# Performance work log

Measured on AMD Instinct MI355X. Metric: run time of the kernel, lower is better.

Reference implementation:

```python
import jax, jax.numpy as jnp
import numpy as np

B, S, D, H, DK, F, L, V = 4, 128, 512, 8, 64, 2048, 2, 32000
N = B * S  # nodes per side (enc and dec each)


def _pe():
    pos = np.arange(S, dtype=np.float32)[:, None]
    div = np.exp(-np.log(10000.0) * np.arange(0, D, 2, dtype=np.float32) / D)
    pe = np.zeros((S, D), dtype=np.float32)
    pe[:, 0::2] = np.sin(pos * div)
    pe[:, 1::2] = np.cos(pos * div)
    return jnp.asarray(np.tile(pe, (B, 1)))  # [N, D]


def _ln(x, g, b, eps=1e-5):
    mu = jnp.mean(x, -1, keepdims=True)
    var = jnp.mean(jnp.square(x - mu), -1, keepdims=True)
    return g * (x - mu) * jax.lax.rsqrt(var + eps) + b


def _edge_attn(q, k, v, src, dst, n_dst):
    # src_dot_dst('k','q','score') then scaled_exp, then src_mul_edge + sum scatter
    s = jnp.sum(k[src] * q[dst], -1, keepdims=True) / np.float32(np.sqrt(DK))  # [E,H,1]
    s = jnp.exp(jnp.clip(s, -10.0, 10.0))
    wv = jax.ops.segment_sum(v[src] * s, dst, num_segments=n_dst)  # [n_dst,H,DK]
    z = jax.ops.segment_sum(s, dst, num_segments=n_dst)            # [n_dst,H,1]
    return wv / z


def _attn_block(x_q, x_kv, Wq, Wk, Wv, Wo, src, dst):
    q = (x_q @ Wq).reshape(-1, H, DK)
    k = (x_kv @ Wk).reshape(-1, H, DK)
    v = (x_kv @ Wv).reshape(-1, H, DK)
    o = _edge_attn(q, k, v, src, dst, x_q.shape[0]).reshape(-1, D)
    return o @ Wo


def _forward(p, src_tok, tgt_tok, ee_src, ee_dst, dd_src, dd_dst, ed_src, ed_dst):
    (src_emb, tgt_emb, enc_Wqkv, enc_Wo, enc_ln1, enc_W1, enc_b1, enc_W2, enc_b2,
     enc_ln2, enc_lnf, dec_Wqkv, dec_Wo, dec_ln1, dec_cWq, dec_cWkv, dec_cWo,
     dec_ln2, dec_W1, dec_b1, dec_W2, dec_b2, dec_ln3, dec_lnf, gen_W, gen_b) = p
    pe = _pe()
    scale = np.float32(np.sqrt(D))
    x_e = src_emb[src_tok].reshape(N, D) * scale + pe  # token + positional embed
    x_d = tgt_emb[tgt_tok].reshape(N, D) * scale + pe
    for l in range(L):  # encoder layers (ee edges)
        xn = _ln(x_e, enc_ln1[l, 0], enc_ln1[l, 1])
        x_e = x_e + _attn_block(xn, xn, enc_Wqkv[l, 0], enc_Wqkv[l, 1], enc_Wqkv[l, 2], enc_Wo[l], ee_src, ee_dst)
        xn = _ln(x_e, enc_ln2[l, 0], enc_ln2[l, 1])
        x_e = x_e + jax.nn.relu(xn @ enc_W1[l] + enc_b1[l]) @ enc_W2[l] + enc_b2[l]
    x_e = _ln(x_e, enc_lnf[0], enc_lnf[1])
    for l in range(L):  # decoder layers: self (dd) then cross (ed)
        xn = _ln(x_d, dec_ln1[l, 0], dec_ln1[l, 1])
        x_d = x_d + _attn_block(xn, xn, dec_Wqkv[l, 0], dec_Wqkv[l, 1], dec_Wqkv[l, 2], dec_Wo[l], dd_src, dd_dst)
        xn = _ln(x_d, dec_ln2[l, 0], dec_ln2[l, 1])
        x_d = x_d + _attn_block(xn, x_e, dec_cWq[l], dec_cWkv[l, 0], dec_cWkv[l, 1], dec_cWo[l], ed_src, ed_dst)
        xn = _ln(x_d, dec_ln3[l, 0], dec_ln3[l, 1])
        x_d = x_d + jax.nn.relu(xn @ dec_W1[l] + dec_b1[l]) @ dec_W2[l] + dec_b2[l]
    x_d = _ln(x_d, dec_lnf[0], dec_lnf[1])
    return jax.nn.log_softmax(x_d @ gen_W + gen_b, axis=-1)  # generator


def setup_inputs():
    key = jax.random.key(0)
    ks = iter(jax.random.split(key, 32))
    w = lambda *shape: jax.random.normal(next(ks), shape, jnp.float32) * 0.02
    lnp = lambda n: jnp.tile(jnp.stack([jnp.ones(D), jnp.zeros(D)])[None], (n, 1, 1))
    # structured edge lists: per-sentence blocks
    i, j = np.meshgrid(np.arange(S), np.arange(S), indexing='ij')  # src pos, dst pos
    base = (np.arange(B)[:, None] * S).astype(np.int32)
    full_s = (base + i.ravel()[None, :]).ravel().astype(np.int32)
    full_d = (base + j.ravel()[None, :]).ravel().astype(np.int32)
    m = i.ravel() <= j.ravel()  # causal mask for dec self-attention
    dd_s = (base + i.ravel()[m][None, :]).ravel().astype(np.int32)
    dd_d = (base + j.ravel()[m][None, :]).ravel().astype(np.int32)
    k1, k2 = jax.random.split(next(ks))
    return dict(
        src_emb=w(V, D), tgt_emb=w(V, D),
        enc_Wqkv=w(L, 3, D, D), enc_Wo=w(L, D, D), enc_ln1=lnp(L),
        enc_W1=w(L, D, F), enc_b1=jnp.zeros((L, F)), enc_W2=w(L, F, D),
        enc_b2=jnp.zeros((L, D)), enc_ln2=lnp(L), enc_lnf=lnp(1)[0],
        dec_Wqkv=w(L, 3, D, D), dec_Wo=w(L, D, D), dec_ln1=lnp(L),
        dec_cWq=w(L, D, D), dec_cWkv=w(L, 2, D, D), dec_cWo=w(L, D, D), dec_ln2=lnp(L),
        dec_W1=w(L, D, F), dec_b1=jnp.zeros((L, F)), dec_W2=w(L, F, D),
        dec_b2=jnp.zeros((L, D)), dec_ln3=lnp(L), dec_lnf=lnp(1)[0],
        gen_W=w(D, V), gen_b=jnp.zeros((V,)),
        src_tok=jax.random.randint(k1, (B, S), 0, V, jnp.int32),
        tgt_tok=jax.random.randint(k2, (B, S), 0, V, jnp.int32),
        ee_src=jnp.asarray(full_s), ee_dst=jnp.asarray(full_d),
        dd_src=jnp.asarray(dd_s), dd_dst=jnp.asarray(dd_d),
        ed_src=jnp.asarray(full_s), ed_dst=jnp.asarray(full_d),
    )


def reference(src_emb, tgt_emb, enc_Wqkv, enc_Wo, enc_ln1, enc_W1, enc_b1, enc_W2,
              enc_b2, enc_ln2, enc_lnf, dec_Wqkv, dec_Wo, dec_ln1, dec_cWq,
              dec_cWkv, dec_cWo, dec_ln2, dec_W1, dec_b1, dec_W2, dec_b2,
              dec_ln3, dec_lnf, gen_W, gen_b, src_tok, tgt_tok, ee_src, ee_dst,
              dd_src, dd_dst, ed_src, ed_dst):
    p = (src_emb, tgt_emb, enc_Wqkv, enc_Wo, enc_ln1, enc_W1, enc_b1, enc_W2,
         enc_b2, enc_ln2, enc_lnf, dec_Wqkv, dec_Wo, dec_ln1, dec_cWq, dec_cWkv,
         dec_cWo, dec_ln2, dec_W1, dec_b1, dec_W2, dec_b2, dec_ln3, dec_lnf,
         gen_W, gen_b)
    return _forward(p, src_tok, tgt_tok, ee_src, ee_dst, dd_src, dd_dst, ed_src, ed_dst)
```

## Files before the change

### kernel.cpp

```cpp
#include <hip/hip_runtime.h>
#include <cstddef>

constexpr int cB = 4, cS = 128, cD = 512, cH = 8, cDK = 64, cF = 2048, cL = 2, cV = 32000;
constexpr int cN = cB * cS;

typedef __attribute__((ext_vector_type(8))) short short8;
typedef __attribute__((ext_vector_type(4))) float f32x4;

__device__ __forceinline__ short f2bf(float x) {
    unsigned u = __builtin_bit_cast(unsigned, x);
    unsigned r = (u + 0x7fffu + ((u >> 16) & 1u)) >> 16;
    return (short)r;
}

__global__ __launch_bounds__(256) void embed_k(const float* __restrict__ emb,
                                               const int* __restrict__ tok,
                                               float* __restrict__ X)
{
    int n = blockIdx.x;
    int tid = threadIdx.x;
    int t = tok[n];
    int pos = n & (cS - 1);
    const float scale = 22.62741699796952f;
    for (int d = tid; d < cD; d += 256) {
        int i2 = d & ~1;
        float div = expf(-9.210340371976184f * (float)i2 / (float)cD);
        float arg = (float)pos * div;
        float p = (d & 1) ? cosf(arg) : sinf(arg);
        X[(long)n * cD + d] = emb[(long)t * cD + d] * scale + p;
    }
// ... 38 lines not shown
    int tid = threadIdx.x;
    const f32x4* s4 = (const f32x4*)s;
#pragma unroll
    for (int i = 0; i < 4; i++) {
        int lin = tid + i * 256;
        int r = lin >> 4, c4 = lin & 15;
        f32x4 v = s4[(long)(k0 + r) * (N >> 2) + (n0 >> 2) + c4];
        t[r][c4 * 4 + 0] = v[0]; t[r][c4 * 4 + 1] = v[1];
        t[r][c4 * 4 + 2] = v[2]; t[r][c4 * 4 + 3] = v[3];
    }
    __syncthreads();
#pragma unroll
    for (int i = 0; i < 2; i++) {
        int lin = tid + i * 256;
        int r = lin >> 3, c8 = lin & 7;
        short8 o;
#pragma unroll
        for (int j = 0; j < 8; j++) o[j] = f2bf(t[c8 * 8 + j][r]);
        *(short8*)&d[(long)(n0 + r) * K + k0 + c8 * 8] = o;
    }
}

template <int MR, int NR, bool LNF>
__global__ __launch_bounds__(256) void gemm_k(
    const short* __restrict__ Abf, const float* __restrict__ Af,
    const float* __restrict__ lng, const float* __restrict__ lnb,
    const short* __restrict__ Bt,
    const float* __restrict__ bias, const float* __restrict__ res,
    float* __restrict__ C, short* __restrict__ Cb,
    int N, int K, int relu, long btStride, long cStride, int swz)
{
    constexpr int BM = MR * 32, BN = NR * 32, BK = 64, PITCH = BK + 8;
    constexpr int ACH = (BM * BK) / (8 * 256);
    constexpr int BCH = (BN * BK) / (8 * 256);
    static_assert(ACH >= 1 && BCH >= 1, "tile too small");
    __shared__ short As[2][BM * PITCH];
    __shared__ short Bs[2][BN * PITCH];
    __shared__ float mu_s[BM], rs_s[BM];
    __shared__ float gb_s[2][512];

    int bx = blockIdx.x, by = blockIdx.y;
    if (swz) {
        int nb = gridDim.x * gridDim.y;
        int bid = by * gridDim.x + bx;
        int w = (bid & 7) * (nb >> 3) + (bid >> 3);
        by = w % gridDim.y; bx = w / gridDim.y;
    }

    const short* Bm = Bt + (long)blockIdx.z * btStride;
    int tid = threadIdx.x;
    int lane = tid & 63, wid = tid >> 6;
    int wr = wid >> 1, wc = wid & 1;
    int m0 = by * BM, n0 = bx * BN;
    int lrow = lane & 15, koff = (lane >> 4) * 8;

    f32x4 acc[MR][NR];
#pragma unroll
    for (int m = 0; m < MR; m++)
#pragma unroll
        for (int n = 0; n < NR; n++) acc[m][n] = f32x4{0.f, 0.f, 0.f, 0.f};

    short8 qa0[ACH], qa1[ACH], qb0[BCH], qb1[BCH];
    f32x4 fa0[LNF ? ACH * 2 : 1], fa1[LNF ? ACH * 2 : 1];

    auto stageA = [&](int k0, short8 (&qa)[ACH], f32x4 (&fa)[LNF ? ACH * 2 : 1]) {
#pragma unroll
        for (int i = 0; i < ACH; i++) {
            int lin = tid + i * 256, r = lin >> 3, c8 = lin & 7;
            if constexpr (LNF) {
                const f32x4* p = (const f32x4*)(Af + (long)(m0 + r) * K + k0 + c8 * 8);
                fa[2 * i] = p[0]; fa[2 * i + 1] = p[1];
            } else {
                qa[i] = *(const short8*)&Abf[(long)(m0 + r) * K + k0 + c8 * 8];
            }
        }
    };
    auto stageB = [&](int k0, short8 (&qb)[BCH]) {
#pragma unroll
        for (int i = 0; i < BCH; i++) {
            int lin = tid + i * 256, r = lin >> 3, c8 = lin & 7;
            qb[i] = *(const short8*)&Bm[(long)(n0 + r) * K + k0 + c8 * 8];
        }
    };
    auto writeT = [&](int buf, int k0, short8 (&qa)[ACH],
                      f32x4 (&fa)[LNF ? ACH * 2 : 1], short8 (&qb)[BCH]) {
#pragma unroll
        for (int i = 0; i < ACH; i++) {
            int lin = tid + i * 256, r = lin >> 3, c8 = lin & 7;
            if constexpr (LNF) {
                float mu = mu_s[r], rs = rs_s[r];
                short8 o;
#pragma unroll
                for (int j = 0; j < 4; j++)
                    o[j] = f2bf((fa[2 * i][j] - mu) * rs * gb_s[0][k0 + c8 * 8 + j] + gb_s[1][k0 + c8 * 8 + j]);
#pragma unroll
                for (int j = 0; j < 4; j++)
                    o[4 + j] = f2bf((fa[2 * i + 1][j] - mu) * rs * gb_s[0][k0 + c8 * 8 + 4 + j] + gb_s[1][k0 + c8 * 8 + 4 + j]);
                *(short8*)&As[buf][r * PITCH + c8 * 8] = o;
            } else {
                *(short8*)&As[buf][r * PITCH + c8 * 8] = qa[i];
            }
        }
#pragma unroll
        for (int i = 0; i < BCH; i++) {
            int lin = tid + i * 256, r = lin >> 3, c8 = lin & 7;
            *(short8*)&Bs[buf][r * PITCH + c8 * 8] = qb[i];
        }
    };
    auto mfmaStep = [&](int buf) {
#pragma unroll
        for (int kk = 0; kk < BK; kk += 32) {
            short8 a[MR], b[NR];
#pragma unroll
            for (int m = 0; m < MR; m++)
                a[m] = *(const short8*)&As[buf][(wr * MR * 16 + m * 16 + lrow) * PITCH + kk + koff];
#pragma unroll
            for (int n = 0; n < NR; n++)
                b[n] = *(const short8*)&Bs[buf][(wc * NR * 16 + n * 16 + lrow) * PITCH + kk + koff];
#pragma unroll
            for (int m = 0; m < MR; m++)
#pragma unroll
                for (int n = 0; n < NR; n++)
                    acc[m][n] = __builtin_amdgcn_mfma_f32_16x16x32_bf16(a[m], b[n], acc[m][n], 0, 0, 0);
        }
    };

    stageA(0, qa0, fa0); stageB(0, qb0);
    if (BK < K) { stageA(BK, qa1, fa1); stageB(BK, qb1); }

    if constexpr (LNF) {
        constexpr int TPR = 256 / BM;
        int r = tid / TPR, sub = tid % TPR;
        const f32x4* row4 = (const f32x4*)(Af + (long)(m0 + r) * K);
        float s = 0.f, s2 = 0.f;
        for (int i = sub; i < (K >> 2); i += TPR) {
            f32x4 v = row4[i];
            s  += v[0] + v[1] + v[2] + v[3];
            s2 += v[0] * v[0] + v[1] * v[1] + v[2] * v[2] + v[3] * v[3];
        }
#pragma unroll
        for (int o = TPR >> 1; o > 0; o >>= 1) {
            s += __shfl_xor(s, o); s2 += __shfl_xor(s2, o);
        }
        if (sub == 0) {
            float mu = s / (float)K;
            float var = s2 / (float)K - mu * mu;
            mu_s[r] = mu; rs_s[r] = rsqrtf(var + 1e-5f);
        }
        for (int i = tid; i < 512; i += 256) {
            gb_s[0][i] = lng[i]; gb_s[1][i] = lnb[i];
        }
        __syncthreads();
    }

    int k0 = 0;
    for (;;) {
        writeT(0, k0, qa0, fa0, qb0);
        __syncthreads();
        if (k0 + 2 * BK < K) { stageA(k0 + 2 * BK, qa0, fa0); stageB(k0 + 2 * BK, qb0); }
        mfmaStep(0);
        k0 += BK; if (k0 >= K) break;

        writeT(1, k0, qa1, fa1, qb1);
        __syncthreads();
        if (k0 + 2 * BK < K) { stageA(k0 + 2 * BK, qa1, fa1); stageB(k0 + 2 * BK, qb1); }
        mfmaStep(1);
        k0 += BK; if (k0 >= K) break;
    }

#pragma unroll
    for (int m = 0; m < MR; m++) {
        int rbase = m0 + wr * MR * 16 + m * 16 + (lane >> 4) * 4;
#pragma unroll
        for (int n = 0; n < NR; n++) {
            int col = n0 + wc * NR * 16 + n * 16 + (lane & 15);
            float bv = bias ? bias[col] : 0.f;
#pragma unroll
            for (int j = 0; j < 4; j++) {
                long row = rbase + j;
                float v = acc[m][n][j] + bv;
                if (res)  v += res[row * N + col];
                if (relu) v = fmaxf(v, 0.f);
                long off = row * N + col + (long)blockIdx.z * cStride;
                if (C)  C[off] = v;
                if (Cb) Cb[off] = f2bf(v);
            }
        }
    }
}

__global__ __launch_bounds__(256) void attn_k(const short* __restrict__ Q,
                                              const short* __restrict__ Km,
                                              const short* __restrict__ Vm,
                                              short* __restrict__ O, int causal)
{
    __shared__ short q_s[64 * 72];
    __shared__ short k_s[128 * 72];
    __shared__ short vt_s[64 * 128];
    __shared__ short p_s[64 * 136];
    __shared__ float z_s[64];

    int tid = threadIdx.x, lane = tid & 63, wid = tid >> 6;
    int lr = lane & 15, lg = lane >> 4;
    int h = blockIdx.x, b = blockIdx.y, dstBase = blockIdx.z * 64;
    const int RS = cH * cDK;
    long qbase = ((long)b * cS + dstBase) * RS + h * cDK;
    long kbase = ((long)b * cS) * RS + h * cDK;

#pragma unroll
    for (int i = 0; i < 2; i++) {
        int lin = tid + i * 256, t = lin >> 3, c8 = lin & 7;
        *(short8*)&q_s[t * 72 + c8 * 8] = *(const short8*)&Q[qbase + (long)t * RS + c8 * 8];
    }
#pragma unroll
    for (int i = 0; i < 4; i++) {
        int lin = tid + i * 256, t = lin >> 3, c8 = lin & 7;
        *(short8*)&k_s[t * 72 + c8 * 8] = *(const short8*)&Km[kbase + (long)t * RS + c8 * 8];
    }
#pragma unroll
    for (int i = 0; i < 4; i++) {
        int lin = tid + i * 256, src = lin >> 3, c8 = lin & 7;
        short8 v = *(const short8*)&Vm[kbase + (long)src * RS + c8 * 8];
#pragma unroll
        for (int j = 0; j < 8; j++) {
            int dk = c8 * 8 + j;
            int g = (src >> 3) ^ (dk >> 3);
            vt_s[dk * 128 + g * 8 + (src & 7)] = v[j];
        }
    }
    __syncthreads();

    f32x4 sacc[8];
#pragma unroll
    for (int n = 0; n < 8; n++) sacc[n] = f32x4{0.f, 0.f, 0.f, 0.f};
#pragma unroll
    for (int kk = 0; kk < 64; kk += 32) {
        short8 a = *(const short8*)&q_s[(wid * 16 + lr) * 72 + kk + lg * 8];
#pragma unroll
        for (int n = 0; n < 8; n++) {
            short8 bf = *(const short8*)&k_s[(n * 16 + lr) * 72 + kk + lg * 8];
            sacc[n] = __builtin_amdgcn_mfma_f32_16x16x32_bf16(a, bf, sacc[n], 0, 0, 0);
        }
    }
    float z[4] = {0.f, 0.f, 0.f, 0.f};
#pragma unroll
    for (int n = 0; n < 8; n++) {
        int src = n * 16 + lr;
#pragma unroll
        for (int j = 0; j < 4; j++) {
            int dst = dstBase + wid * 16 + lg * 4 + j;
            float s = sacc[n][j] * 0.125f;
            s = __expf(fminf(fmaxf(s, -10.f), 10.f));
            if (causal && src > dst) s = 0.f;
            sacc[n][j] = s;
            z[j] += s;
        }
    }
#pragma unroll
    for (int j = 0; j < 4; j++) {
        z[j] += __shfl_xor(z[j], 1); z[j] += __shfl_xor(z[j], 2);
        z[j] += __shfl_xor(z[j], 4); z[j] += __shfl_xor(z[j], 8);
    }
#pragma unroll
    for (int n = 0; n < 8; n++) {
        int src = n * 16 + lr;
#pragma unroll
        for (int j = 0; j < 4; j++)
            p_s[(wid * 16 + lg * 4 + j) * 136 + src] = f2bf(sacc[n][j]);
    }
    if (lr == 0) {
#pragma unroll
        for (int j = 0; j < 4; j++) z_s[wid * 16 + lg * 4 + j] = z[j];
    }
    __syncthreads();

    f32x4 oacc[4];
#pragma unroll
    for (int n = 0; n < 4; n++) oacc[n] = f32x4{0.f, 0.f, 0.f, 0.f};
#pragma unroll
    for (int kk = 0; kk < 128; kk += 32) {
        int dkr = wid * 16 + lr;
        int g = ((kk >> 3) + lg) ^ (dkr >> 3);
        short8 a = *(const short8*)&vt_s[dkr * 128 + g * 8];
#pragma unroll
        for (int n = 0; n < 4; n++) {
            short8 bf = *(const short8*)&p_s[(n * 16 + lr) * 136 + kk + lg * 8];
            oacc[n] = __builtin_amdgcn_mfma_f32_16x16x32_bf16(a, bf, oacc[n], 0, 0, 0);
        }
    }
#pragma unroll
    for (int n = 0; n < 4; n++) {
        int dl = n * 16 + lr;
        float zz = z_s[dl];
#pragma unroll
        for (int j = 0; j < 4; j++) {
            int dk = wid * 16 + lg * 4 + j;
            O[qbase + (long)dl * RS + dk] = f2bf(oacc[n][j] / zz);
        }
    }
}

__global__ __launch_bounds__(256) void lsm_k(float* __restrict__ X)
{
    __shared__ float rm[256], rs[256];
    int row = blockIdx.x, tid = threadIdx.x;
    f32x4* x4 = (f32x4*)(X + (long)row * cV);
    constexpr int NV = cV / 4;

    float m = -1e30f, s = 0.f;
    for (int i = tid; i < NV; i += 256) {
        f32x4 v = x4[i];
        float cm = fmaxf(fmaxf(v[0], v[1]), fmaxf(v[2], v[3]));
        float nm = fmaxf(m, cm);
        s = s * __expf(m - nm)
          + __expf(v[0] - nm) + __expf(v[1] - nm)
          + __expf(v[2] - nm) + __expf(v[3] - nm);
        m = nm;
    }
    rm[tid] = m; rs[tid] = s;
    __syncthreads();
// ... 35 lines not shown
    const float* dec_ln1  = (const float*)d_in[13];
    const float* dec_cWq  = (const float*)d_in[14];
    const float* dec_cWkv = (const float*)d_in[15];
    const float* dec_cWo  = (const float*)d_in[16];
    const float* dec_ln2  = (const float*)d_in[17];
    const float* dec_W1   = (const float*)d_in[18];
    const float* dec_b1   = (const float*)d_in[19];
    const float* dec_W2   = (const float*)d_in[20];
    const float* dec_b2   = (const float*)d_in[21];
    const float* dec_ln3  = (const float*)d_in[22];
    const float* dec_lnf  = (const float*)d_in[23];
    const float* gen_W    = (const float*)d_in[24];
    const float* gen_b    = (const float*)d_in[25];
    const int* src_tok    = (const int*)d_in[26];
    const int* tgt_tok    = (const int*)d_in[27];

    const long ND = (long)cN * cD;
    const long DD = (long)cD * cD;
    const long DF = (long)cD * cF;

    float* x_e = (float*)d_ws;
    float* x_d = x_e + ND;

    short* qkvb  = (short*)(x_d + ND);
    short* ob_bf = qkvb + 3 * ND;
    short* hb_bf = ob_bf + ND;
    short* kvc   = hb_bf + (long)cN * cF;
    short* xn_bf = kvc + 4 * ND;
    short* wDD  = xn_bf + ND;
    short* wDF  = wDD + 24 * DD;
    short* wFD  = wDF + 4 * DF;
    short* genT = wFD + 4 * DF;

    {
        TCP p{};
        int i = 0;
        for (int j = 0; j < 6; j++) p.s[i++] = enc_Wqkv + (long)j * DD;
        for (int j = 0; j < 2; j++) p.s[i++] = enc_Wo   + (long)j * DD;
        for (int j = 0; j < 6; j++) p.s[i++] = dec_Wqkv + (long)j * DD;
        for (int j = 0; j < 2; j++) p.s[i++] = dec_Wo   + (long)j * DD;
        for (int j = 0; j < 2; j++) p.s[i++] = dec_cWq  + (long)j * DD;
        for (int j = 0; j < 4; j++) p.s[i++] = dec_cWkv + (long)j * DD;
        for (int j = 0; j < 2; j++) p.s[i++] = dec_cWo  + (long)j * DD;
        tconv_k<<<dim3(cD / 64, cD / 64, 24), 256, 0, stream>>>(p, wDD, cD, cD);
    }
    {
        TCP p{};
        p.s[0] = enc_W1; p.s[1] = enc_W1 + DF; p.s[2] = dec_W1; p.s[3] = dec_W1 + DF;
        tconv_k<<<dim3(cF / 64, cD / 64, 4), 256, 0, stream>>>(p, wDF, cD, cF);
    }
    {
        TCP p{};
        p.s[0] = enc_W2; p.s[1] = enc_W2 + DF; p.s[2] = dec_W2; p.s[3] = dec_W2 + DF;
        tconv_k<<<dim3(cD / 64, cF / 64, 4), 256, 0, stream>>>(p, wFD, cF, cD);
    }
    {
        TCP p{};
        p.s[0] = gen_W;
        tconv_k<<<dim3(cV / 64, cD / 64, 1), 256, 0, stream>>>(p, genT, cD, cV);
    }

    embed_k<<<cN, 256, 0, stream>>>(src_emb, src_tok, x_e);
    embed_k<<<cN, 256, 0, stream>>>(tgt_emb, tgt_tok, x_d);

    dim3 gDD11(cD / 32, cN / 32);
    dim3 gFFN1(cF / 64, cN / 64);
    dim3 gAttn(cH, cB, 2);

    for (int l = 0; l < cL; l++) {
        gemm_k<1, 1, true><<<dim3(cD / 32, cN / 32, 3), 256, 0, stream>>>(
            nullptr, x_e, enc_ln1 + (long)(2 * l) * cD, enc_ln1 + (long)(2 * l + 1) * cD,
            wDD + (long)(3 * l) * DD, nullptr, nullptr, nullptr, qkvb,
            cD, cD, 0, DD, ND, 0);
        attn_k<<<gAttn, 256, 0, stream>>>(qkvb, qkvb + ND, qkvb + 2 * ND, ob_bf, 0);
        gemm_k<1, 1, false><<<gDD11, 256, 0, stream>>>(
            ob_bf, nullptr, nullptr, nullptr, wDD + (long)(6 + l) * DD,
            nullptr, x_e, x_e, nullptr, cD, cD, 0, 0, 0, 0);
        gemm_k<2, 2, true><<<gFFN1, 256, 0, stream>>>(
            nullptr, x_e, enc_ln2 + (long)(2 * l) * cD, enc_ln2 + (long)(2 * l + 1) * cD,
            wDF + (long)l * DF, enc_b1 + (long)l * cF, nullptr, nullptr, hb_bf,
            cF, cD, 1, 0, 0, 0);
        gemm_k<1, 1, false><<<gDD11, 256, 0, stream>>>(
            hb_bf, nullptr, nullptr, nullptr, wFD + (long)l * DF,
            enc_b2 + (long)l * cD, x_e, x_e, nullptr, cD, cF, 0, 0, 0, 0);
    }

    gemm_k<1, 1, true><<<dim3(cD / 32, cN / 32, 4), 256, 0, stream>>>(
        nullptr, x_e, enc_lnf, enc_lnf + cD,
        wDD + 18 * DD, nullptr, nullptr, nullptr, kvc,
        cD, cD, 0, DD, ND, 0);

    for (int l = 0; l < cL; l++) {
        gemm_k<1, 1, true><<<dim3(cD / 32, cN / 32, 3), 256, 0, stream>>>(
            nullptr, x_d, dec_ln1 + (long)(2 * l) * cD, dec_ln1 + (long)(2 * l + 1) * cD,
            wDD + (long)(8 + 3 * l) * DD, nullptr, nullptr, nullptr, qkvb,
            cD, cD, 0, DD, ND, 0);
        attn_k<<<gAttn, 256, 0, stream>>>(qkvb, qkvb + ND, qkvb + 2 * ND, ob_bf, 1);
        gemm_k<1, 1, false><<<gDD11, 256, 0, stream>>>(
            ob_bf, nullptr, nullptr, nullptr, wDD + (long)(14 + l) * DD,
            nullptr, x_d, x_d, nullptr, cD, cD, 0, 0, 0, 0);

        gemm_k<1, 1, true><<<gDD11, 256, 0, stream>>>(
            nullptr, x_d, dec_ln2 + (long)(2 * l) * cD, dec_ln2 + (long)(2 * l + 1) * cD,
            wDD + (long)(16 + l) * DD, nullptr, nullptr, nullptr, qkvb,
            cD, cD, 0, 0, 0, 0);
        attn_k<<<gAttn, 256, 0, stream>>>(qkvb, kvc + (long)(2 * l) * ND,
                                          kvc + (long)(2 * l + 1) * ND, ob_bf, 0);
        gemm_k<1, 1, false><<<gDD11, 256, 0, stream>>>(
            ob_bf, nullptr, nullptr, nullptr, wDD + (long)(22 + l) * DD,
            nullptr, x_d, x_d, nullptr, cD, cD, 0, 0, 0, 0);

        gemm_k<2, 2, true><<<gFFN1, 256, 0, stream>>>(
            nullptr, x_d, dec_ln3 + (long)(2 * l) * cD, dec_ln3 + (long)(2 * l + 1) * cD,
            wDF + (long)(2 + l) * DF, dec_b1 + (long)l * cF, nullptr, nullptr, hb_bf,
            cF, cD, 1, 0, 0, 0);
        gemm_k<1, 1, false><<<gDD11, 256, 0, stream>>>(
            hb_bf, nullptr, nullptr, nullptr, wFD + (long)(2 + l) * DF,
            dec_b2 + (long)l * cD, x_d, x_d, nullptr, cD, cF, 0, 0, 0, 0);
    }

    ln_k<<<cN, 256, 0, stream>>>(x_d, dec_lnf, dec_lnf + cD, xn_bf);
    gemm_k<4, 2, false><<<dim3(cV / 64, cN / 128), 256, 0, stream>>>(
        xn_bf, nullptr, nullptr, nullptr, genT, gen_b, nullptr,
        (float*)d_out, nullptr, cV, cD, 0, 0, 0, 1);
    lsm_k<<<cN, 256, 0, stream>>>((float*)d_out);
}
```

Baseline: 377.8 us.

## Fuse LN+QKV projection into attention, split-K 512-thread GEMMs, 32x32 MFMA generator

```diff
diff --git a/kernel.cpp b/kernel.cpp
--- a/kernel.cpp
+++ b/kernel.cpp
@@ -4,8 +4,9 @@
 constexpr int cB = 4, cS = 128, cD = 512, cH = 8, cDK = 64, cF = 2048, cL = 2, cV = 32000;
 constexpr int cN = cB * cS;
 
-typedef __attribute__((ext_vector_type(8))) short short8;
-typedef __attribute__((ext_vector_type(4))) float f32x4;
+typedef __attribute__((ext_vector_type(8)))  short short8;
+typedef __attribute__((ext_vector_type(4)))  float f32x4;
+typedef __attribute__((ext_vector_type(16))) float f32x16;
 
 __device__ __forceinline__ short f2bf(float x) {
     unsigned u = __builtin_bit_cast(unsigned, x);
@@ -90,114 +91,35 @@
 }
 
 template <int MR, int NR, bool LNF>
-__global__ __launch_bounds__(256) void gemm_k(
+__global__ __launch_bounds__(512) void gemm8_k(
     const short* __restrict__ Abf, const float* __restrict__ Af,
     const float* __restrict__ lng, const float* __restrict__ lnb,
     const short* __restrict__ Bt,
     const float* __restrict__ bias, const float* __restrict__ res,
     float* __restrict__ C, short* __restrict__ Cb,
-    int N, int K, int relu, long btStride, long cStride, int swz)
+    int N, int K, int relu, long btStride, long cStride)
 {
-    constexpr int BM = MR * 32, BN = NR * 32, BK = 64, PITCH = BK + 8;
-    constexpr int ACH = (BM * BK) / (8 * 256);
-    constexpr int BCH = (BN * BK) / (8 * 256);
+    constexpr int BM = MR * 32, BN = NR * 32, PITCH = 136;
+    constexpr int ACH = (BM * 128) / (8 * 512);
+    constexpr int BCH = (BN * 128) / (8 * 512);
     static_assert(ACH >= 1 && BCH >= 1, "tile too small");
     __shared__ short As[2][BM * PITCH];
     __shared__ short Bs[2][BN * PITCH];
+    __shared__ float red[4][64][MR * NR * 4];
     __shared__ float mu_s[BM], rs_s[BM];
-    __shared__ float gb_s[2][512];
-
-    int bx = blockIdx.x, by = blockIdx.y;
-    if (swz) {
-        int nb = gridDim.x * gridDim.y;
-        int bid = by * gridDim.x + bx;
-        int w = (bid & 7) * (nb >> 3) + (bid >> 3);
-        by = w % gridDim.y; bx = w / gridDim.y;
-    }
+    __shared__ float gb_s[2][LNF ? 512 : 8];
 
     const short* Bm = Bt + (long)blockIdx.z * btStride;
     int tid = threadIdx.x;
     int lane = tid & 63, wid = tid >> 6;
-    int wr = wid >> 1, wc = wid & 1;
-    int m0 = by * BM, n0 = bx * BN;
+    int grp = wid >> 2, quad = wid & 3;
+    int wr = quad >> 1, wc = quad & 1;
+    int m0 = blockIdx.y * BM, n0 = blockIdx.x * BN;
     int lrow = lane & 15, koff = (lane >> 4) * 8;
-
-    f32x4 acc[MR][NR];
-#pragma unroll
-    for (int m = 0; m < MR; m++)
-#pragma unroll
-        for (int n = 0; n < NR; n++) acc[m][n] = f32x4{0.f, 0.f, 0.f, 0.f};
-
-    short8 qa0[ACH], qa1[ACH], qb0[BCH], qb1[BCH];
-    f32x4 fa0[LNF ? ACH * 2 : 1], fa1[LNF ? ACH * 2 : 1];
-
-    auto stageA = [&](int k0, short8 (&qa)[ACH], f32x4 (&fa)[LNF ? ACH * 2 : 1]) {
-#pragma unroll
-        for (int i = 0; i < ACH; i++) {
-            int lin = tid + i * 256, r = lin >> 3, c8 = lin & 7;
-            if constexpr (LNF) {
-                const f32x4* p = (const f32x4*)(Af + (long)(m0 + r) * K + k0 + c8 * 8);
-                fa[2 * i] = p[0]; fa[2 * i + 1] = p[1];
-            } else {
-                qa[i] = *(const short8*)&Abf[(long)(m0 + r) * K + k0 + c8 * 8];
-            }
-        }
-    };
-    auto stageB = [&](int k0, short8 (&qb)[BCH]) {
-#pragma unroll
-        for (int i = 0; i < BCH; i++) {
-            int lin = tid + i * 256, r = lin >> 3, c8 = lin & 7;
-            qb[i] = *(const short8*)&Bm[(long)(n0 + r) * K + k0 + c8 * 8];
-        }
-    };
-    auto writeT = [&](int buf, int k0, short8 (&qa)[ACH],
-                      f32x4 (&fa)[LNF ? ACH * 2 : 1], short8 (&qb)[BCH]) {
-#pragma unroll
-        for (int i = 0; i < ACH; i++) {
-            int lin = tid + i * 256, r = lin >> 3, c8 = lin & 7;
-            if constexpr (LNF) {
-                float mu = mu_s[r], rs = rs_s[r];
-                short8 o;
-#pragma unroll
-                for (int j = 0; j < 4; j++)
-                    o[j] = f2bf((fa[2 * i][j] - mu) * rs * gb_s[0][k0 + c8 * 8 + j] + gb_s[1][k0 + c8 * 8 + j]);
-#pragma unroll
-                for (int j = 0; j < 4; j++)
-                    o[4 + j] = f2bf((fa[2 * i + 1][j] - mu) * rs * gb_s[0][k0 + c8 * 8 + 4 + j] + gb_s[1][k0 + c8 * 8 + 4 + j]);
-                *(short8*)&As[buf][r * PITCH + c8 * 8] = o;
-            } else {
-                *(short8*)&As[buf][r * PITCH + c8 * 8] = qa[i];
-            }
-        }
-#pragma unroll
-        for (int i = 0; i < BCH; i++) {
-            int lin = tid + i * 256, r = lin >> 3, c8 = lin & 7;
-            *(short8*)&Bs[buf][r * PITCH + c8 * 8] = qb[i];
-        }
-    };
-    auto mfmaStep = [&](int buf) {
-#pragma unroll
-        for (int kk = 0; kk < BK; kk += 32) {
-            short8 a[MR], b[NR];
-#pragma unroll
-            for (int m = 0; m < MR; m++)
-                a[m] = *(const short8*)&As[buf][(wr * MR * 16 + m * 16 + lrow) * PITCH + kk + koff];
-#pragma unroll
-            for (int n = 0; n < NR; n++)
-                b[n] = *(const short8*)&Bs[buf][(wc * NR * 16 + n * 16 + lrow) * PITCH + kk + koff];
-#pragma unroll
-            for (int m = 0; m < MR; m++)
-#pragma unroll
-                for (int n = 0; n < NR; n++)
-                    acc[m][n] = __builtin_amdgcn_mfma_f32_16x16x32_bf16(a[m], b[n], acc[m][n], 0, 0, 0);
-        }
-    };
-
-    stageA(0, qa0, fa0); stageB(0, qb0);
-    if (BK < K) { stageA(BK, qa1, fa1); stageB(BK, qb1); }
+    const int Kh = K >> 1;
 
     if constexpr (LNF) {
-        constexpr int TPR = 256 / BM;
+        constexpr int TPR = 512 / BM;
         int r = tid / TPR, sub = tid % TPR;
         const f32x4* row4 = (const f32x4*)(Af + (long)(m0 + r) * K);
         float s = 0.f, s2 = 0.f;
@@ -215,155 +137,465 @@
             float var = s2 / (float)K - mu * mu;
             mu_s[r] = mu; rs_s[r] = rsqrtf(var + 1e-5f);
         }
-        for (int i = tid; i < 512; i += 256) {
-            gb_s[0][i] = lng[i]; gb_s[1][i] = lnb[i];
-        }
-        __syncthreads();
-    }
-
-    int k0 = 0;
+        for (int i = tid; i < 512; i += 512) { gb_s[0][i] = lng[i]; gb_s[1][i] = lnb[i]; }
+        __syncthreads();
+    }
+
+    f32x4 acc[MR][NR];
+#pragma unroll
+    for (int m = 0; m < MR; m++)
+#pragma unroll
+        for (int n = 0; n < NR; n++) acc[m][n] = f32x4{0.f, 0.f, 0.f, 0.f};
+
+    short8 qa0[ACH], qa1[ACH], qb0[BCH], qb1[BCH];
+
+    auto stage = [&](int step, short8 (&qa)[ACH], short8 (&qb)[BCH]) {
+#pragma unroll
+        for (int i = 0; i < ACH; i++) {
+            int lin = tid + i * 512, r = lin >> 4, c8 = lin & 15;
+            int kg = (c8 < 8) ? (step * 64 + c8 * 8) : (Kh + step * 64 + (c8 - 8) * 8);
+            if constexpr (LNF) {
+                const f32x4* p = (const f32x4*)(Af + (long)(m0 + r) * K + kg);
+                f32x4 f0 = p[0], f1 = p[1];
+                float mu = mu_s[r], rs = rs_s[r];
+                short8 o;
+#pragma unroll
+                for (int j = 0; j < 4; j++)
+                    o[j] = f2bf((f0[j] - mu) * rs * gb_s[0][kg + j] + gb_s[1][kg + j]);
+#pragma unroll
+                for (int j = 0; j < 4; j++)
+                    o[4 + j] = f2bf((f1[j] - mu) * rs * gb_s[0][kg + 4 + j] + gb_s[1][kg + 4 + j]);
+                qa[i] = o;
+            } else {
+                qa[i] = *(const short8*)&Abf[(long)(m0 + r) * K + kg];
+            }
+        }
+#pragma unroll
+        for (int i = 0; i < BCH; i++) {
+            int lin = tid + i * 512, r = lin >> 4, c8 = lin & 15;
+            int kg = (c8 < 8) ? (step * 64 + c8 * 8) : (Kh + step * 64 + (c8 - 8) * 8);
+            qb[i] = *(const short8*)&Bm[(long)(n0 + r) * K + kg];
+        }
+    };
+    auto writeT = [&](int buf, short8 (&qa)[ACH], short8 (&qb)[BCH]) {
+#pragma unroll
+        for (int i = 0; i < ACH; i++) {
+            int lin = tid + i * 512, r = lin >> 4, c8 = lin & 15;
+            *(short8*)&As[buf][r * PITCH + c8 * 8] = qa[i];
+        }
+#pragma unroll
+        for (int i = 0; i < BCH; i++) {
+            int lin = tid + i * 512, r = lin >> 4, c8 = lin & 15;
+            *(short8*)&Bs[buf][r * PITCH + c8 * 8] = qb[i];
+        }
+    };
+    auto mfmaStep = [&](int buf) {
+#pragma unroll
+        for (int kk2 = 0; kk2 < 2; kk2++) {
+            int kk = grp * 64 + kk2 * 32;
+            short8 a[MR], b[NR];
+#pragma unroll
+            for (int m = 0; m < MR; m++)
+                a[m] = *(const short8*)&As[buf][(wr * MR * 16 + m * 16 + lrow) * PITCH + kk + koff];
+#pragma unroll
+            for (int n = 0; n < NR; n++)
+                b[n] = *(const short8*)&Bs[buf][(wc * NR * 16 + n * 16 + lrow) * PITCH + kk + koff];
+#pragma unroll
+            for (int m = 0; m < MR; m++)
+#pragma unroll
+                for (int n = 0; n < NR; n++)
+                    acc[m][n] = __builtin_amdgcn_mfma_f32_16x16x32_bf16(a[m], b[n], acc[m][n], 0, 0, 0);
+        }
+    };
+
+    const int steps = K >> 7;
+    stage(0, qa0, qb0);
+    if (steps > 1) stage(1, qa1, qb1);
+
+    int st = 0;
     for (;;) {
-        writeT(0, k0, qa0, fa0, qb0);
-        __syncthreads();
-        if (k0 + 2 * BK < K) { stageA(k0 + 2 * BK, qa0, fa0); stageB(k0 + 2 * BK, qb0); }
+        writeT(0, qa0, qb0);
+        __syncthreads();
+        if (st + 2 < steps) stage(st + 2, qa0, qb0);
         mfmaStep(0);
-        k0 += BK; if (k0 >= K) break;
-
-        writeT(1, k0, qa1, fa1, qb1);
-        __syncthreads();
-        if (k0 + 2 * BK < K) { stageA(k0 + 2 * BK, qa1, fa1); stageB(k0 + 2 * BK, qb1); }
+        st++; if (st >= steps) break;
+
+        writeT(1, qa1, qb1);
+        __syncthreads();
+        if (st + 2 < steps) stage(st + 2, qa1, qb1);
         mfmaStep(1);
-        k0 += BK; if (k0 >= K) break;
-    }
-
-#pragma unroll
-    for (int m = 0; m < MR; m++) {
-        int rbase = m0 + wr * MR * 16 + m * 16 + (lane >> 4) * 4;
-#pragma unroll
-        for (int n = 0; n < NR; n++) {
-            int col = n0 + wc * NR * 16 + n * 16 + (lane & 15);
-            float bv = bias ? bias[col] : 0.f;
-#pragma unroll
-            for (int j = 0; j < 4; j++) {
-                long row = rbase + j;
-                float v = acc[m][n][j] + bv;
-                if (res)  v += res[row * N + col];
-                if (relu) v = fmaxf(v, 0.f);
-                long off = row * N + col + (long)blockIdx.z * cStride;
-                if (C)  C[off] = v;
-                if (Cb) Cb[off] = f2bf(v);
-            }
-        }
-    }
-}
-
-__global__ __launch_bounds__(256) void attn_k(const short* __restrict__ Q,
-                                              const short* __restrict__ Km,
-                                              const short* __restrict__ Vm,
-                                              short* __restrict__ O, int causal)
+        st++; if (st >= steps) break;
+    }
+
+    __syncthreads();
+    if (grp == 1) {
+#pragma unroll
+        for (int m = 0; m < MR; m++)
+#pragma unroll
+            for (int n = 0; n < NR; n++)
+#pragma unroll
+                for (int j = 0; j < 4; j++)
+                    red[quad][lane][(m * NR + n) * 4 + j] = acc[m][n][j];
+    }
+    __syncthreads();
+    if (grp == 0) {
+#pragma unroll
+        for (int m = 0; m < MR; m++) {
+            int rbase = m0 + wr * MR * 16 + m * 16 + (lane >> 4) * 4;
+#pragma unroll
+            for (int n = 0; n < NR; n++) {
+                int col = n0 + wc * NR * 16 + n * 16 + (lane & 15);
+                float bv = bias ? bias[col] : 0.f;
+#pragma unroll
+                for (int j = 0; j < 4; j++) {
+                    long row = rbase + j;
+                    float v = acc[m][n][j] + red[quad][lane][(m * NR + n) * 4 + j] + bv;
+                    if (res)  v += res[row * N + col];
+                    if (relu) v = fmaxf(v, 0.f);
+                    long off = row * N + col + (long)blockIdx.z * cStride;
+                    if (C)  C[off] = v;
+                    if (Cb) Cb[off] = f2bf(v);
+                }
+            }
+        }
+    }
+}
+
+template <bool SELF>
+__global__ __launch_bounds__(256) void fattn_k(
+    const float* __restrict__ X, const float* __restrict__ lng,
+    const float* __restrict__ lnb, const short* __restrict__ W,
+    const short* __restrict__ KV, short* __restrict__ O, int causal)
 {
-    __shared__ short q_s[64 * 72];
-    __shared__ short k_s[128 * 72];
-    __shared__ short vt_s[64 * 128];
-    __shared__ short p_s[64 * 136];
-    __shared__ float z_s[64];
+    constexpr int NB = SELF ? 192 : 64;
+    constexpr int NR = NB / 32;
+    constexpr int PITCH = 72;
+    constexpr int ACH = 4;
+    constexpr int BCH = NB * 64 / 2048;
+
+    __shared__ float mu_s[128], rs_s[128], gb0[512], gb1[512], z_s[64];
+    __shared__ short Q_s[128 * PITCH];
+    __shared__ short K_s[128 * PITCH];
+    __shared__ short VT_s[64 * 128];
+    __shared__ __align__(16) char uni[(2 * 128 + 2 * NB) * PITCH * 2];
+    short* AsB = (short*)uni;
+    short* BsB = AsB + 2 * 128 * PITCH;
+    short* P_s = (short*)uni;
 
     int tid = threadIdx.x, lane = tid & 63, wid = tid >> 6;
     int lr = lane & 15, lg = lane >> 4;
-    int h = blockIdx.x, b = blockIdx.y, dstBase = blockIdx.z * 64;
-    const int RS = cH * cDK;
-    long qbase = ((long)b * cS + dstBase) * RS + h * cDK;
-    long kbase = ((long)b * cS) * RS + h * cDK;
-
-#pragma unroll
-    for (int i = 0; i < 2; i++) {
-        int lin = tid + i * 256, t = lin >> 3, c8 = lin & 7;
-        *(short8*)&q_s[t * 72 + c8 * 8] = *(const short8*)&Q[qbase + (long)t * RS + c8 * 8];
-    }
-#pragma unroll
-    for (int i = 0; i < 4; i++) {
-        int lin = tid + i * 256, t = lin >> 3, c8 = lin & 7;
-        *(short8*)&k_s[t * 72 + c8 * 8] = *(const short8*)&Km[kbase + (long)t * RS + c8 * 8];
-    }
-#pragma unroll
-    for (int i = 0; i < 4; i++) {
-        int lin = tid + i * 256, src = lin >> 3, c8 = lin & 7;
-        short8 v = *(const short8*)&Vm[kbase + (long)src * RS + c8 * 8];
-#pragma unroll
-        for (int j = 0; j < 8; j++) {
-            int dk = c8 * 8 + j;
-            int g = (src >> 3) ^ (dk >> 3);
-            vt_s[dk * 128 + g * 8 + (src & 7)] = v[j];
+    int h = blockIdx.x, b = blockIdx.y;
+    int wr = wid >> 1, wc = wid & 1;
+    int lrow = lr, koff = lg * 8;
+
+    {
+        int r = tid >> 1, sub = tid & 1;
+        const f32x4* row4 = (const f32x4*)(X + ((long)(b * cS + r)) * cD);
+        float s = 0.f, s2 = 0.f;
+        for (int i = sub; i < 128; i += 2) {
+            f32x4 v = row4[i];
+            s  += v[0] + v[1] + v[2] + v[3];
+            s2 += v[0] * v[0] + v[1] * v[1] + v[2] * v[2] + v[3] * v[3];
+        }
+        s += __shfl_xor(s, 1); s2 += __shfl_xor(s2, 1);
+        if (sub == 0) {
+            float mu = s * (1.f / 512.f);
+            float var = s2 * (1.f / 512.f) - mu * mu;
+            mu_s[r] = mu; rs_s[r] = rsqrtf(var + 1e-5f);
+        }
+        for (int i = tid; i < 512; i += 256) { gb0[i] = lng[i]; gb1[i] = lnb[i]; }
+        __syncthreads();
+    }
+
+    f32x4 acc[4][NR];
+#pragma unroll
+    for (int m = 0; m < 4; m++)
+#pragma unroll
+        for (int n = 0; n < NR; n++) acc[m][n] = f32x4{0.f, 0.f, 0.f, 0.f};
+
+    short8 qa[ACH], qb[BCH];
+    auto stage = [&](int k0) {
+#pragma unroll
+        for (int i = 0; i < ACH; i++) {
+            int lin = tid + i * 256, r = lin >> 3, c8 = lin & 7;
+            int kg = k0 + c8 * 8;
+            const f32x4* p = (const f32x4*)(X + ((long)(b * cS + r)) * cD + kg);
+            f32x4 f0 = p[0], f1 = p[1];
+            float mu = mu_s[r], rs = rs_s[r];
+            short8 o;
+#pragma unroll
+            for (int j = 0; j < 4; j++) o[j]     = f2bf((f0[j] - mu) * rs * gb0[kg + j] + gb1[kg + j]);
+#pragma unroll
+            for (int j = 0; j < 4; j++) o[4 + j] = f2bf((f1[j] - mu) * rs * gb0[kg + 4 + j] + gb1[kg + 4 + j]);
+            qa[i] = o;
+        }
+#pragma unroll
+        for (int i = 0; i < BCH; i++) {
+            int lin = tid + i * 256, r = lin >> 3, c8 = lin & 7;
+            long wrow = (long)((r >> 6) * 512 + h * 64 + (r & 63));
+            qb[i] = *(const short8*)&W[wrow * 512 + k0 + c8 * 8];
+        }
+    };
+    auto writeT = [&](int buf) {
+        short* Asb = AsB + buf * 128 * PITCH;
+        short* Bsb = BsB + buf * NB * PITCH;
+#pragma unroll
+        for (int i = 0; i < ACH; i++) {
+            int lin = tid + i * 256, r = lin >> 3, c8 = lin & 7;
+            *(short8*)&Asb[r * PITCH + c8 * 8] = qa[i];
+        }
+#pragma unroll
+        for (int i = 0; i < BCH; i++) {
+            int lin = tid + i * 256, r = lin >> 3, c8 = lin & 7;
+            *(short8*)&Bsb[r * PITCH + c8 * 8] = qb[i];
+        }
+    };
+    auto mfmaStep = [&](int buf) {
+        short* Asb = AsB + buf * 128 * PITCH;
+        short* Bsb = BsB + buf * NB * PITCH;
+#pragma unroll
+        for (int kk = 0; kk < 64; kk += 32) {
+            short8 a[4], bb[NR];
+#pragma unroll
+            for (int m = 0; m < 4; m++)
+                a[m] = *(const short8*)&Asb[(wr * 64 + m * 16 + lrow) * PITCH + kk + koff];
+#pragma unroll
+            for (int n = 0; n < NR; n++)
+                bb[n] = *(const short8*)&Bsb[(wc * (NB / 2) + n * 16 + lrow) * PITCH + kk + koff];
+#pragma unroll
+            for (int m = 0; m < 4; m++)
+#pragma unroll
+                for (int n = 0; n < NR; n++)
+                    acc[m][n] = __builtin_amdgcn_mfma_f32_16x16x32_bf16(a[m], bb[n], acc[m][n], 0, 0, 0);
+        }
+    };
+
+    stage(0);
+    for (int st = 0; st < 8; st++) {
+        int buf = st & 1;
+        writeT(buf);
+        __syncthreads();
+        if (st + 1 < 8) stage((st + 1) * 64);
+        mfmaStep(buf);
+    }
+
+#pragma unroll
+    for (int m = 0; m < 4; m++) {
+        int r4 = wr * 64 + m * 16 + lg * 4;
+#pragma unroll
+        for (int n = 0; n < NR; n++) {
+            int col = wc * (NB / 2) + n * 16 + lr;
+#pragma unroll
+            for (int j = 0; j < 4; j++) {
+                int row = r4 + j;
+                short v = f2bf(acc[m][n][j]);
+                if (SELF) {
+                    if (col < 64)       Q_s[row * PITCH + col] = v;
+                    else if (col < 128) K_s[row * PITCH + (col - 64)] = v;
+                    else {
+                        int dk = col - 128;
+                        int g = (row >> 3) ^ (dk >> 3);
+                        VT_s[dk * 128 + g * 8 + (row & 7)] = v;
+                    }
+                } else {
+                    Q_s[row * PITCH + col] = v;
+                }
+            }
+        }
+    }
+    if (!SELF) {
+        const short* Vp = KV + (long)cN * cD;
+        long kb = ((long)b * cS) * cD + h * 64;
+#pragma unroll
+        for (int i = 0; i < 4; i++) {
+            int lin = tid + i * 256, t = lin >> 3, c8 = lin & 7;
+            *(short8*)&K_s[t * PITCH + c8 * 8] = *(const short8*)&KV[kb + (long)t * cD + c8 * 8];
+            short8 v = *(const short8*)&Vp[kb + (long)t * cD + c8 * 8];
+#pragma unroll
+            for (int j = 0; j < 8; j++) {
+                int dk = c8 * 8 + j;
+                int g = (t >> 3) ^ (dk >> 3);
+                VT_s[dk * 128 + g * 8 + (t & 7)] = v[j];
+            }
         }
     }
     __syncthreads();
 
-    f32x4 sacc[8];
-#pragma unroll
-    for (int n = 0; n < 8; n++) sacc[n] = f32x4{0.f, 0.f, 0.f, 0.f};
-#pragma unroll
-    for (int kk = 0; kk < 64; kk += 32) {
-        short8 a = *(const short8*)&q_s[(wid * 16 + lr) * 72 + kk + lg * 8];
+    for (int h2 = 0; h2 < 2; h2++) {
+        f32x4 sacc[8];
+#pragma unroll
+        for (int n = 0; n < 8; n++) sacc[n] = f32x4{0.f, 0.f, 0.f, 0.f};
+#pragma unroll
+        for (int kk = 0; kk < 64; kk += 32) {
+            short8 a = *(const short8*)&Q_s[(h2 * 64 + wid * 16 + lr) * PITCH + kk + lg * 8];
+#pragma unroll
+            for (int n = 0; n < 8; n++) {
+                short8 bf = *(const short8*)&K_s[(n * 16 + lr) * PITCH + kk + lg * 8];
+                sacc[n] = __builtin_amdgcn_mfma_f32_16x16x32_bf16(a, bf, sacc[n], 0, 0, 0);
+            }
+        }
+        float z[4] = {0.f, 0.f, 0.f, 0.f};
 #pragma unroll
         for (int n = 0; n < 8; n++) {
-            short8 bf = *(const short8*)&k_s[(n * 16 + lr) * 72 + kk + lg * 8];
-            sacc[n] = __builtin_amdgcn_mfma_f32_16x16x32_bf16(a, bf, sacc[n], 0, 0, 0);
-        }
-    }
-    float z[4] = {0.f, 0.f, 0.f, 0.f};
-#pragma unroll
-    for (int n = 0; n < 8; n++) {
-        int src = n * 16 + lr;
+            int src = n * 16 + lr;
+#pragma unroll
+            for (int j = 0; j < 4; j++) {
+                int dst = h2 * 64 + wid * 16 + lg * 4 + j;
+                float s = sacc[n][j] * 0.125f;
+                s = __expf(fminf(fmaxf(s, -10.f), 10.f));
+                if (causal && src > dst) s = 0.f;
+                sacc[n][j] = s;
+                z[j] += s;
+            }
+        }
 #pragma unroll
         for (int j = 0; j < 4; j++) {
-            int dst = dstBase + wid * 16 + lg * 4 + j;
-            float s = sacc[n][j] * 0.125f;
-            s = __expf(fminf(fmaxf(s, -10.f), 10.f));
-            if (causal && src > dst) s = 0.f;
-            sacc[n][j] = s;
-            z[j] += s;
-        }
-    }
-#pragma unroll
-    for (int j = 0; j < 4; j++) {
-        z[j] += __shfl_xor(z[j], 1); z[j] += __shfl_xor(z[j], 2);
-        z[j] += __shfl_xor(z[j], 4); z[j] += __shfl_xor(z[j], 8);
-    }
-#pragma unroll
-    for (int n = 0; n < 8; n++) {
-        int src = n * 16 + lr;
-#pragma unroll
-        for (int j = 0; j < 4; j++)
-            p_s[(wid * 16 + lg * 4 + j) * 136 + src] = f2bf(sacc[n][j]);
-    }
-    if (lr == 0) {
-#pragma unroll
-        for (int j = 0; j < 4; j++) z_s[wid * 16 + lg * 4 + j] = z[j];
-    }
-    __syncthreads();
-
-    f32x4 oacc[4];
-#pragma unroll
-    for (int n = 0; n < 4; n++) oacc[n] = f32x4{0.f, 0.f, 0.f, 0.f};
-#pragma unroll
-    for (int kk = 0; kk < 128; kk += 32) {
-        int dkr = wid * 16 + lr;
-        int g = ((kk >> 3) + lg) ^ (dkr >> 3);
-        short8 a = *(const short8*)&vt_s[dkr * 128 + g * 8];
+            z[j] += __shfl_xor(z[j], 1); z[j] += __shfl_xor(z[j], 2);
+            z[j] += __shfl_xor(z[j], 4); z[j] += __shfl_xor(z[j], 8);
+        }
+#pragma unroll
+        for (int n = 0; n < 8; n++) {
+            int src = n * 16 + lr;
+#pragma unroll
+            for (int j = 0; j < 4; j++)
+                P_s[(wid * 16 + lg * 4 + j) * 136 + src] = f2bf(sacc[n][j]);
+        }
+        if (lr == 0) {
+#pragma unroll
+            for (int j = 0; j < 4; j++) z_s[wid * 16 + lg * 4 + j] = z[j];
+        }
+        __syncthreads();
+
+        f32x4 oacc[4];
+#pragma unroll
+        for (int n = 0; n < 4; n++) oacc[n] = f32x4{0.f, 0.f, 0.f, 0.f};
+#pragma unroll
+        for (int kk = 0; kk < 128; kk += 32) {
+            int dkr = wid * 16 + lr;
+            int g = ((kk >> 3) + lg) ^ (dkr >> 3);
+            short8 a = *(const short8*)&VT_s[dkr * 128 + g * 8];
+#pragma unroll
+            for (int n = 0; n < 4; n++) {
+                short8 bf = *(const short8*)&P_s[(n * 16 + lr) * 136 + kk + lg * 8];
+                oacc[n] = __builtin_amdgcn_mfma_f32_16x16x32_bf16(a, bf, oacc[n], 0, 0, 0);
+            }
+        }
 #pragma unroll
         for (int n = 0; n < 4; n++) {
-            short8 bf = *(const short8*)&p_s[(n * 16 + lr) * 136 + kk + lg * 8];
-            oacc[n] = __builtin_amdgcn_mfma_f32_16x16x32_bf16(a, bf, oacc[n], 0, 0, 0);
-        }
-    }
-#pragma unroll
-    for (int n = 0; n < 4; n++) {
-        int dl = n * 16 + lr;
-        float zz = z_s[dl];
-#pragma unroll
-        for (int j = 0; j < 4; j++) {
-            int dk = wid * 16 + lg * 4 + j;
-            O[qbase + (long)dl * RS + dk] = f2bf(oacc[n][j] / zz);
+            int dl = n * 16 + lr;
+            float zz = z_s[dl];
+#pragma unroll
+            for (int j = 0; j < 4; j++) {
+                int dk = wid * 16 + lg * 4 + j;
+                O[((long)(b * cS + h2 * 64 + dl)) * cD + h * 64 + dk] = f2bf(oacc[n][j] / zz);
+            }
+        }
+        __syncthreads();
+    }
+}
+
+__global__ __launch_bounds__(256) void gen32_k(
+    const short* __restrict__ A, const short* __restrict__ Bt,
+    const float* __restrict__ bias, float* __restrict__ C, int N, int K)
+{
+    constexpr int PITCH = 72;
+    constexpr int ACH = 4, BCH = 4;
+    __shared__ short As[2][128 * PITCH];
+    __shared__ short Bs[2][128 * PITCH];
+
+    int bx = blockIdx.x, by = blockIdx.y;
+    {
+        int nb = gridDim.x * gridDim.y;
+        int bid = by * gridDim.x + bx;
+        int w = (bid & 7) * (nb >> 3) + (bid >> 3);
+        by = w % gridDim.y; bx = w / gridDim.y;
+    }
+    int tid = threadIdx.x;
+    int lane = tid & 63, wid = tid >> 6;
+    int wr = wid >> 1, wc = wid & 1;
+    int m0 = by * 128, n0 = bx * 128;
+    int l31 = lane & 31, l5 = lane >> 5;
+
+    f32x16 acc[2][2];
+#pragma unroll
+    for (int m = 0; m < 2; m++)
+#pragma unroll
+        for (int n = 0; n < 2; n++)
+#pragma unroll
+            for (int r = 0; r < 16; r++) acc[m][n][r] = 0.f;
+
+    short8 qa0[ACH], qa1[ACH], qb0[BCH], qb1[BCH];
+    auto stage = [&](int k0, short8 (&qa)[ACH], short8 (&qb)[BCH]) {
+#pragma unroll
+        for (int i = 0; i < ACH; i++) {
+            int lin = tid + i * 256, r = lin >> 3, c8 = lin & 7;
+            qa[i] = *(const short8*)&A[(long)(m0 + r) * K + k0 + c8 * 8];
+        }
+#pragma unroll
+        for (int i = 0; i < BCH; i++) {
+            int lin = tid + i * 256, r = lin >> 3, c8 = lin & 7;
+            qb[i] = *(const short8*)&Bt[(long)(n0 + r) * K + k0 + c8 * 8];
+        }
+    };
+    auto writeT = [&](int buf, short8 (&qa)[ACH], short8 (&qb)[BCH]) {
+#pragma unroll
+        for (int i = 0; i < ACH; i++) {
+            int lin = tid + i * 256, r = lin >> 3, c8 = lin & 7;
+            *(short8*)&As[buf][r * PITCH + c8 * 8] = qa[i];
+        }
+#pragma unroll
+        for (int i = 0; i < BCH; i++) {
+            int lin = tid + i * 256, r = lin >> 3, c8 = lin & 7;
+            *(short8*)&Bs[buf][r * PITCH + c8 * 8] = qb[i];
+        }
+    };
+    auto mfmaStep = [&](int buf) {
+#pragma unroll
+        for (int kk = 0; kk < 64; kk += 16) {
+            short8 a[2], b[2];
+#pragma unroll
+            for (int m = 0; m < 2; m++)
+                a[m] = *(const short8*)&As[buf][(wr * 64 + m * 32 + l31) * PITCH + kk + l5 * 8];
+#pragma unroll
+            for (int n = 0; n < 2; n++)
+                b[n] = *(const short8*)&Bs[buf][(wc * 64 + n * 32 + l31) * PITCH + kk + l5 * 8];
+#pragma unroll
+            for (int m = 0; m < 2; m++)
+#pragma unroll
+                for (int n = 0; n < 2; n++)
+                    acc[m][n] = __builtin_amdgcn_mfma_f32_32x32x16_bf16(a[m], b[n], acc[m][n], 0, 0, 0);
+        }
+    };
+
+    const int steps = K >> 6;
+    stage(0, qa0, qb0);
+    stage(64, qa1, qb1);
+    int st = 0;
+    for (;;) {
+        writeT(0, qa0, qb0);
+        __syncthreads();
+        if (st + 2 < steps) stage((st + 2) * 64, qa0, qb0);
+        mfmaStep(0);
+        st++; if (st >= steps) break;
+
+        writeT(1, qa1, qb1);
+        __syncthreads();
+        if (st + 2 < steps) stage((st + 2) * 64, qa1, qb1);
+        mfmaStep(1);
+        st++; if (st >= steps) break;
+    }
+
+#pragma unroll
+    for (int m = 0; m < 2; m++) {
+#pragma unroll
+        for (int n = 0; n < 2; n++) {
+            int col = n0 + wc * 64 + n * 32 + l31;
+            float bv = bias[col];
+#pragma unroll
+            for (int r = 0; r < 16; r++) {
+                int row = m0 + wr * 64 + m * 32 + (r & 3) + 8 * (r >> 2) + 4 * l5;
+                C[(long)row * N + col] = acc[m][n][r] + bv;
+            }
         }
     }
 }
@@ -445,8 +677,7 @@
     float* x_e = (float*)d_ws;
     float* x_d = x_e + ND;
 
-    short* qkvb  = (short*)(x_d + ND);
-    short* ob_bf = qkvb + 3 * ND;
+    short* ob_bf = (short*)(x_d + ND);
     short* hb_bf = ob_bf + ND;
     short* kvc   = hb_bf + (long)cN * cF;
     short* xn_bf = kvc + 4 * ND;
@@ -486,65 +717,56 @@
     embed_k<<<cN, 256, 0, stream>>>(src_emb, src_tok, x_e);
     embed_k<<<cN, 256, 0, stream>>>(tgt_emb, tgt_tok, x_d);
 
-    dim3 gDD11(cD / 32, cN / 32);
+    dim3 gDD(cD / 32, cN / 32);
     dim3 gFFN1(cF / 64, cN / 64);
-    dim3 gAttn(cH, cB, 2);
+    dim3 gAttn(cH, cB);
 
     for (int l = 0; l < cL; l++) {
-        gemm_k<1, 1, true><<<dim3(cD / 32, cN / 32, 3), 256, 0, stream>>>(
-            nullptr, x_e, enc_ln1 + (long)(2 * l) * cD, enc_ln1 + (long)(2 * l + 1) * cD,
-            wDD + (long)(3 * l) * DD, nullptr, nullptr, nullptr, qkvb,
-            cD, cD, 0, DD, ND, 0);
-        attn_k<<<gAttn, 256, 0, stream>>>(qkvb, qkvb + ND, qkvb + 2 * ND, ob_bf, 0);
-        gemm_k<1, 1, false><<<gDD11, 256, 0, stream>>>(
+        fattn_k<true><<<gAttn, 256, 0, stream>>>(
+            x_e, enc_ln1 + (long)(2 * l) * cD, enc_ln1 + (long)(2 * l + 1) * cD,
+            wDD + (long)(3 * l) * DD, nullptr, ob_bf, 0);
+        gemm8_k<1, 1, false><<<gDD, 512, 0, stream>>>(
             ob_bf, nullptr, nullptr, nullptr, wDD + (long)(6 + l) * DD,
-            nullptr, x_e, x_e, nullptr, cD, cD, 0, 0, 0, 0);
-        gemm_k<2, 2, true><<<gFFN1, 256, 0, stream>>>(
+            nullptr, x_e, x_e, nullptr, cD, cD, 0, 0, 0);
+        gemm8_k<2, 2, true><<<gFFN1, 512, 0, stream>>>(
             nullptr, x_e, enc_ln2 + (long)(2 * l) * cD, enc_ln2 + (long)(2 * l + 1) * cD,
             wDF + (long)l * DF, enc_b1 + (long)l * cF, nullptr, nullptr, hb_bf,
-            cF, cD, 1, 0, 0, 0);
-        gemm_k<1, 1, false><<<gDD11, 256, 0, stream>>>(
+            cF, cD, 1, 0, 0);
+        gemm8_k<1, 1, false><<<gDD, 512, 0, stream>>>(
             hb_bf, nullptr, nullptr, nullptr, wFD + (long)l * DF,
-            enc_b2 + (long)l * cD, x_e, x_e, nullptr, cD, cF, 0, 0, 0, 0);
-    }
-
-    gemm_k<1, 1, true><<<dim3(cD / 32, cN / 32, 4), 256, 0, stream>>>(
+            enc_b2 + (long)l * cD, x_e, x_e, nullptr, cD, cF, 0, 0, 0);
+    }
+
+    gemm8_k<1, 1, true><<<dim3(cD / 32, cN / 32, 4), 512, 0, stream>>>(
         nullptr, x_e, enc_lnf, enc_lnf + cD,
-        wDD + 18 * DD, nullptr, nullptr, nullptr, kvc,
-        cD, cD, 0, DD, ND, 0);
+        wDD + 18 * DD, nullptr, nullptr, nullptr, kvc, cD, cD, 0, DD, ND);
 
     for (int l = 0; l < cL; l++) {
-        gemm_k<1, 1, true><<<dim3(cD / 32, cN / 32, 3), 256, 0, stream>>>(
-            nullptr, x_d, dec_ln1 + (long)(2 * l) * cD, dec_ln1 + (long)(2 * l + 1) * cD,
-            wDD + (long)(8 + 3 * l) * DD, nullptr, nullptr, nullptr, qkvb,
-            cD, cD, 0, DD, ND, 0);
-        attn_k<<<gAttn, 256, 0, stream>>>(qkvb, qkvb + ND, qkvb + 2 * ND, ob_bf, 1);
-        gemm_k<1, 1, false><<<gDD11, 256, 0, stream>>>(
+        fattn_k<true><<<gAttn, 256, 0, stream>>>(
+            x_d, dec_ln1 + (long)(2 * l) * cD, dec_ln1 + (long)(2 * l + 1) * cD,
+            wDD + (long)(8 + 3 * l) * DD, nullptr, ob_bf, 1);
+        gemm8_k<1, 1, false><<<gDD, 512, 0, stream>>>(
             ob_bf, nullptr, nullptr, nullptr, wDD + (long)(14 + l) * DD,
-            nullptr, x_d, x_d, nullptr, cD, cD, 0, 0, 0, 0);
-
-        gemm_k<1, 1, true><<<gDD11, 256, 0, stream>>>(
-            nullptr, x_d, dec_ln2 + (long)(2 * l) * cD, dec_ln2 + (long)(2 * l + 1) * cD,
-            wDD + (long)(16 + l) * DD, nullptr, nullptr, nullptr, qkvb,
-            cD, cD, 0, 0, 0, 0);
-        attn_k<<<gAttn, 256, 0, stream>>>(qkvb, kvc + (long)(2 * l) * ND,
-                                          kvc + (long)(2 * l + 1) * ND, ob_bf, 0);
-        gemm_k<1, 1, false><<<gDD11, 256, 0, stream>>>(
+            nullptr, x_d, x_d, nullptr, cD, cD, 0, 0, 0);
+
+        fattn_k<false><<<gAttn, 256, 0, stream>>>(
+            x_d, dec_ln2 + (long)(2 * l) * cD, dec_ln2 + (long)(2 * l + 1) * cD,
+            wDD + (long)(16 + l) * DD, kvc + (long)(2 * l) * ND, ob_bf, 0);
+        gemm8_k<1, 1, false><<<gDD, 512, 0, stream>>>(
             ob_bf, nullptr, nullptr, nullptr, wDD + (long)(22 + l) * DD,
-            nullptr, x_d, x_d, nullptr, cD, cD, 0, 0, 0, 0);
-
-        gemm_k<2, 2, true><<<gFFN1, 256, 0, stream>>>(
+            nullptr, x_d, x_d, nullptr, cD, cD, 0, 0, 0);
+
+        gemm8_k<2, 2, true><<<gFFN1, 512, 0, stream>>>(
             nullptr, x_d, dec_ln3 + (long)(2 * l) * cD, dec_ln3 + (long)(2 * l + 1) * cD,
             wDF + (long)(2 + l) * DF, dec_b1 + (long)l * cF, nullptr, nullptr, hb_bf,
-            cF, cD, 1, 0, 0, 0);
-        gemm_k<1, 1, false><<<gDD11, 256, 0, stream>>>(
+            cF, cD, 1, 0, 0);
+        gemm8_k<1, 1, false><<<gDD, 512, 0, stream>>>(
             hb_bf, nullptr, nullptr, nullptr, wFD + (long)(2 + l) * DF,
-            dec_b2 + (long)l * cD, x_d, x_d, nullptr, cD, cF, 0, 0, 0, 0);
+            dec_b2 + (long)l * cD, x_d, x_d, nullptr, cD, cF, 0, 0, 0);
     }
 
     ln_k<<<cN, 256, 0, stream>>>(x_d, dec_lnf, dec_lnf + cD, xn_bf);
-    gemm_k<4, 2, false><<<dim3(cV / 64, cN / 128), 256, 0, stream>>>(
-        xn_bf, nullptr, nullptr, nullptr, genT, gen_b, nullptr,
-        (float*)d_out, nullptr, cV, cD, 0, 0, 0, 1);
+    gen32_k<<<dim3(cV / 128, cN / 128), 256, 0, stream>>>(
+        xn_bf, genT, gen_b, (float*)d_out, cV, cD);
     lsm_k<<<cN, 256, 0, stream>>>((float*)d_out);
 }
```

After: 450.8 us. 1.19x slower.
